# Kernel optimization log

Hardware: AMD Instinct MI355X
Metric: run time of the kernel (lower is better)

## Reference

```python
import jax, jax.numpy as jnp
import numpy as np

# wav2vec2 feature-extractor conv stack config: (kernel, stride) per layer, 512 channels
CONV_CFG = [(10, 5), (3, 2), (3, 2), (3, 2), (3, 2), (2, 2), (2, 2)]
C = 512
PROJ = 256
HID = 128
NCLS = 5
N_WORDS = 64
B = 8
L = 40000


def _conv1d(h, w, stride):
    # h: [B, Cin, T], w: [Cout, Cin, K]
    return jax.lax.conv_general_dilated(
        h, w, window_strides=(stride,), padding='VALID',
        dimension_numbers=('NCH', 'OIH', 'NCH'))


def setup_inputs() -> dict:
    key = jax.random.key(0)
    ks = jax.random.split(key, 16)
    x = jax.random.normal(ks[0], (B, L), dtype=jnp.float32)
    word_ids = jax.random.randint(ks[1], (B,), 0, N_WORDS)
    convs = {}
    cin = 1
    for i, (k, s) in enumerate(CONV_CFG):
        fan = cin * k
        convs[f'conv{i}'] = jax.random.normal(ks[2 + i], (C, cin, k), dtype=jnp.float32) / np.sqrt(fan)
        cin = C
    gn_scale = jnp.ones((C,), dtype=jnp.float32)
    gn_bias = jnp.zeros((C,), dtype=jnp.float32)
    proj_w = jax.random.normal(ks[9], (PROJ, C), dtype=jnp.float32) / np.sqrt(C)
    proj_b = jnp.zeros((PROJ,), dtype=jnp.float32)
    cls_w1 = jax.random.normal(ks[10], (N_WORDS, PROJ, HID), dtype=jnp.float32) / np.sqrt(PROJ)
    cls_b1 = jnp.zeros((N_WORDS, HID), dtype=jnp.float32)
    cls_w2 = jax.random.normal(ks[11], (N_WORDS, HID, NCLS), dtype=jnp.float32) / np.sqrt(HID)
    cls_b2 = jnp.zeros((N_WORDS, NCLS), dtype=jnp.float32)
    return dict(x=x, word_ids=word_ids, gn_scale=gn_scale, gn_bias=gn_bias,
                proj_w=proj_w, proj_b=proj_b, cls_w1=cls_w1, cls_b1=cls_b1,
                cls_w2=cls_w2, cls_b2=cls_b2, **convs)


def _forward(x, convs, gn_scale, gn_bias, proj_w, proj_b, cls_w1, cls_b1, cls_w2, cls_b2, word_ids):
    h = x[:, None, :]  # [B,1,L]
    for i, (k, s) in enumerate(CONV_CFG):
        h = _conv1d(h, convs[i], s)
        if i == 0:
            # wav2vec2 group-norm: groups == channels -> per-channel norm over time
            mu = jnp.mean(h, axis=-1, keepdims=True)
            var = jnp.var(h, axis=-1, keepdims=True)
            h = (h - mu) * jax.lax.rsqrt(var + 1e-5)
            h = h * gn_scale[None, :, None] + gn_bias[None, :, None]
        h = jax.nn.gelu(h)
    feat = jnp.mean(h, axis=-1)                          # [B, 512] mean-pool over time
    feat = jax.nn.relu(feat @ proj_w.T + proj_b)         # [B, 256] (dropout = identity in eval)
    w1 = cls_w1[word_ids]                                # [B, 256, 128] routed gather
    h1 = jax.nn.relu(jnp.einsum('bd,bdh->bh', feat, w1) + cls_b1[word_ids])
    out = jnp.einsum('bh,bho->bo', h1, cls_w2[word_ids]) + cls_b2[word_ids]  # [B, 5]
    return out


def reference(x, word_ids, gn_scale, gn_bias, proj_w, proj_b, cls_w1, cls_b1, cls_w2, cls_b2,
              conv0, conv1, conv2, conv3, conv4, conv5, conv6):
    convs = [conv0, conv1, conv2, conv3, conv4, conv5, conv6]
    return _forward(x, convs, gn_scale, gn_bias, proj_w, proj_b,
                    cls_w1, cls_b1, cls_w2, cls_b2, word_ids)
```

## Files before the change

### kernel.cpp

```cpp
#include <hip/hip_runtime.h>
#include <hip/hip_bf16.h>

typedef unsigned short u16;
typedef short bf16x8 __attribute__((ext_vector_type(8)));
typedef float f32x4 __attribute__((ext_vector_type(4)));

#define CC 512

__device__ __forceinline__ float gelu_tanh(float x) {
    float x3 = x * x * x;
    float z  = 0.7978845608028654f * (x + 0.044715f * x3);
    float e  = __expf(2.0f * z);
    float th = 1.0f - 2.0f / (e + 1.0f);
    return 0.5f * x * (1.0f + th);
}

__device__ __forceinline__ u16 f2bf(float f) {
    union { float f; unsigned u; } v; v.f = f;
    unsigned r = v.u + 0x7fff + ((v.u >> 16) & 1);
    return (u16)(r >> 16);
}
__device__ __forceinline__ float bf2f(u16 h) {
    union { unsigned u; float f; } v; v.u = ((unsigned)h) << 16; return v.f;
}

__global__ __launch_bounds__(256) void conv0_stats(
    const float* __restrict__ x, const float* __restrict__ w0,
    float* __restrict__ part) {
    const int chunk = blockIdx.x, b = blockIdx.y;
    const int t0 = chunk * 250;
    __shared__ float xs[250 * 5 + 10];
    __shared__ float w0s[512 * 10];
    for (int i = threadIdx.x; i < 1260; i += 256) {
        int gi = t0 * 5 + i;
        xs[i] = (gi < 40000) ? x[b * 40000 + gi] : 0.0f;
    }
    for (int i = threadIdx.x; i < 5120; i += 256) w0s[i] = w0[i];
    __syncthreads();
    const int nt = min(250, 7999 - t0);
    for (int cc = 0; cc < 2; ++cc) {
        const int c = threadIdx.x * 2 + cc;
        const float* wr = &w0s[c * 10];
        float s = 0.0f, q = 0.0f;
        for (int t = 0; t < nt; ++t) {
            float a = 0.0f;
#pragma unroll
            for (int j = 0; j < 10; ++j) a = fmaf(wr[j], xs[t * 5 + j], a);
            s += a; q += a * a;
        }
        float* p = part + ((size_t)(b * 512 + c) * 32 + chunk) * 2;
        p[0] = s; p[1] = q;
    }
}

__global__ __launch_bounds__(256) void stats_finalize(
    const float* __restrict__ part, float* __restrict__ stats) {
    const int row = blockIdx.x * 256 + threadIdx.x;
    const float* p = part + (size_t)row * 32 * 2;
    float s = 0.0f, q = 0.0f;
    for (int k = 0; k < 32; ++k) { s += p[k * 2]; q += p[k * 2 + 1]; }
    float mean = s / 7999.0f;
    float var  = fmaxf(q / 7999.0f - mean * mean, 0.0f);
    stats[row * 2]     = mean;
    stats[row * 2 + 1] = rsqrtf(var + 1e-5f);
}

__global__ __launch_bounds__(256) void conv0_apply(
    const float* __restrict__ x, const float* __restrict__ w0,
    const float* __restrict__ stats, const float* __restrict__ gsc,
    const float* __restrict__ gbi, u16* __restrict__ actG) {
    const int t0 = blockIdx.x * 32, b = blockIdx.y;
    __shared__ float xs[32 * 5 + 16];
    __shared__ float w0s[512 * 10];
    __shared__ float A[512], Bb[512];
    for (int i = threadIdx.x; i < 170; i += 256) {
        int gi = t0 * 5 + i;
        xs[i] = (gi < 40000) ? x[b * 40000 + gi] : 0.0f;
    }
    for (int i = threadIdx.x; i < 5120; i += 256) w0s[i] = w0[i];
    for (int c = threadIdx.x; c < 512; c += 256) {
        float m = stats[(b * 512 + c) * 2], r = stats[(b * 512 + c) * 2 + 1];
        float a = r * gsc[c];
        A[c] = a; Bb[c] = gbi[c] - m * a;
    }
    __syncthreads();
    const int c0 = (threadIdx.x & 63) * 8;
    const int wv = threadIdx.x >> 6;
    u16 res[8][8];
#pragma unroll
    for (int q = 0; q < 8; ++q) {
        const int c = c0 + q;
        float wreg[10];
#pragma unroll
        for (int j = 0; j < 10; ++j) wreg[j] = w0s[c * 10 + j];
        const float Ar = A[c], Br = Bb[c];
#pragma unroll
        for (int u = 0; u < 8; ++u) {
            const int tt = wv * 8 + u;
            float a = 0.0f;
#pragma unroll
            for (int j = 0; j < 10; ++j) a = fmaf(wreg[j], xs[tt * 5 + j], a);
            res[u][q] = f2bf(gelu_tanh(fmaf(a, Ar, Br)));
        }
    }
#pragma unroll
    for (int u = 0; u < 8; ++u) {
        const int t = t0 + wv * 8 + u;
        union { u16 s[8]; uint4 v; } pk;
#pragma unroll
        for (int q = 0; q < 8; ++q) pk.s[q] = (t < 7999) ? res[u][q] : (u16)0;
        *(uint4*)(actG + ((size_t)b * 8320 + t) * 512 + c0) = pk.v;
    }
}

template <int K, int NL>
struct WtBatch { const float* src[NL]; u16* dst[NL]; };

template <int K, int NL>
__global__ __launch_bounds__(256) void wt_transform(WtBatch<K, NL> a) {
    constexpr int WROW = 32 * K + 8;
    const int cit = blockIdx.x, cob = blockIdx.y, l = blockIdx.z;
    const float* w = a.src[l];
    u16* dst = a.dst[l] + ((size_t)(cob * 16 + cit)) * 128 * WROW;
    for (int idx = threadIdx.x; idx < 128 * WROW; idx += 256) {
        const int co = idx / WROW, e = idx - co * WROW;
        u16 hi = 0;
        if (e < 32 * K) {
            const int j = e >> 5, ci = e & 31;
            hi = f2bf(w[((size_t)(cob * 128 + co) * 512 + cit * 32 + ci) * K + j]);
        }
        dst[idx] = hi;
    }
}

template <int K, int TT>
__global__ __launch_bounds__(256, (TT == 128 ? 2 : 3)) void conv_mfma(
    const u16* __restrict__ act, int capIn,
    const u16* __restrict__ wt,
    u16* __restrict__ outAct, int capOut, int tbShift) {
    constexpr int WROW = 32 * K + 8;
    constexpr int XH   = TT + 8;
    constexpr int TF   = TT / 32;
    constexpr int NXCH = XH * 8;
    constexpr int NWCH = 128 * WROW / 8;

    __shared__ __align__(16) u16 Xs[XH * 64];
    __shared__ __align__(16) u16 Ws[128 * WROW];

    const int tid  = threadIdx.x;
    const int lane = tid & 63;
    const int wv   = tid >> 6;
    const int wco  = wv >> 1, wtt = wv & 1;
    const int l15  = lane & 15, l16 = lane >> 4;

    const int flat = blockIdx.x;
    const int xcd  = flat & 7, cob = (flat >> 3) & 3;
    const int G    = xcd + (flat >> 5) * 8;
    const int t_b  = G & ((1 << tbShift) - 1);
    const int b    = G >> tbShift;
    const int t0   = t_b * TT;
    const int x0   = t0 * 2;

    const char* abase = (const char*)(act + (size_t)b * capIn * 512);
    const u16*  wbase = wt + (size_t)cob * (16 * 128 * WROW);

    auto stageX = [&](int cit) {
        const char* asl = abase + cit * 64;
#pragma unroll
        for (int k = 0; k < (NXCH + 255) / 256; ++k) {
            const int cb = wv * 64 + k * 256;
            if (cb < NXCH) {
                const int c  = cb + lane;
                const int xh = c >> 3;
                const int li = ((c & 7) * 16) ^ ((xh & 7) << 4);
                int x = x0 + 2 * xh + (li >> 6);
                x = min(x, capIn - 1);
                __builtin_amdgcn_global_load_lds(
                    (const __attribute__((address_space(1))) void*)(asl + (size_t)x * 1024 + (li & 63)),
                    (__attribute__((address_space(3))) void*)((char*)&Xs[0] + cb * 16),
                    16, 0, 0);
            }
        }
    };
    auto stageW = [&](int cit) {
        const char* p = (const char*)(wbase + (size_t)cit * 128 * WROW);
#pragma unroll
        for (int k = 0; k < (NWCH + 255) / 256; ++k) {
            const int cb = wv * 64 + k * 256;
            if (cb < NWCH)
                __builtin_amdgcn_global_load_lds(
                    (const __attribute__((address_space(1))) void*)(p + (size_t)(cb + lane) * 16),
                    (__attribute__((address_space(3))) void*)((char*)&Ws[0] + cb * 16),
                    16, 0, 0);
        }
    };

    int xoff[K][TF];
    int woff[K][4];
#pragma unroll
    for (int j = 0; j < K; ++j) {
#pragma unroll
        for (int tf = 0; tf < TF; ++tf) {
            const int tl = wtt * (TT / 2) + tf * 16 + l15;
            const int xl = 2 * tl + j;
            const int xh = xl >> 1, p = xl & 1;
            xoff[j][tf] = xh * 128 + ((p * 64 + l16 * 16) ^ ((xh & 7) << 4));
        }
#pragma unroll
        for (int cf = 0; cf < 4; ++cf)
            woff[j][cf] = (wco * 64 + cf * 16 + l15) * WROW + j * 32 + l16 * 8;
    }

    f32x4 acc[4][TF] = {};

    stageX(0); stageW(0);
    __syncthreads();

#pragma unroll 1
    for (int cit = 0; cit < 16; ++cit) {
        bf16x8 xr[K][TF], wr[K][4];
#pragma unroll
        for (int j = 0; j < K; ++j) {
#pragma unroll
            for (int tf = 0; tf < TF; ++tf)
                xr[j][tf] = *(const bf16x8*)((const char*)&Xs[0] + xoff[j][tf]);
#pragma unroll
            for (int cf = 0; cf < 4; ++cf)
                wr[j][cf] = *(const bf16x8*)(&Ws[0] + woff[j][cf]);
        }
        __syncthreads();
        if (cit < 15) { stageX(cit + 1); stageW(cit + 1); }
#pragma unroll
        for (int j = 0; j < K; ++j)
#pragma unroll
            for (int cf = 0; cf < 4; ++cf)
#pragma unroll
                for (int tf = 0; tf < TF; ++tf)
                    acc[cf][tf] = __builtin_amdgcn_mfma_f32_16x16x32_bf16(
                        wr[j][cf], xr[j][tf], acc[cf][tf], 0, 0, 0);
        __syncthreads();
    }

    u16* ob = outAct + (size_t)b * capOut * 512;
#pragma unroll
    for (int cf = 0; cf < 4; ++cf) {
#pragma unroll
        for (int tf = 0; tf < TF; ++tf) {
            const int tG  = t0 + wtt * (TT / 2) + tf * 16 + l15;
            const int coG = cob * 128 + wco * 64 + cf * 16 + l16 * 4;
            union { u16 s[4]; uint2 v; } pk;
#pragma unroll
            for (int r = 0; r < 4; ++r)
                pk.s[r] = f2bf(gelu_tanh(acc[cf][tf][r]));
            *(uint2*)(ob + (size_t)tG * 512 + coG) = pk.v;
        }
    }
}

__global__ __launch_bounds__(512) void feat_proj_kernel(
    const u16* __restrict__ act, int cap,
    const float* __restrict__ pw, const float* __restrict__ pb,
    float* __restrict__ pfeat) {
    const int b = blockIdx.x;
    __shared__ float feat[CC];
    const int c = threadIdx.x;
    float s = 0.0f;
    for (int t = 0; t < 124; ++t) s += bf2f(act[((size_t)b * cap + t) * 512 + c]);
    feat[c] = s * (1.0f / 124.0f);
    __syncthreads();
    if (threadIdx.x < 256) {
        const int j = threadIdx.x;
        const float* wr = pw + (size_t)j * CC;
        float acc = pb[j];
        for (int cc = 0; cc < CC; ++cc) acc = fmaf(feat[cc], wr[cc], acc);
        pfeat[b * 256 + j] = fmaxf(acc, 0.0f);
    }
}

__global__ __launch_bounds__(128) void cls_kernel(
    const float* __restrict__ pfeat, const int* __restrict__ wid,
    const float* __restrict__ w1, const float* __restrict__ b1,
    const float* __restrict__ w2, const float* __restrict__ b2,
    float* __restrict__ out) {
    const int b = blockIdx.x;
    const int id = wid[b];
    __shared__ float pf[256], h1[128];
    for (int d = threadIdx.x; d < 256; d += 128) pf[d] = pfeat[b * 256 + d];
    __syncthreads();
    {
        const int hh = threadIdx.x;
        const float* w1p = w1 + (size_t)id * 256 * 128;
        float s = b1[id * 128 + hh];
        for (int d = 0; d < 256; ++d) s = fmaf(pf[d], w1p[d * 128 + hh], s);
        h1[hh] = fmaxf(s, 0.0f);
    }
    __syncthreads();
    if (threadIdx.x < 5) {
        const float* w2p = w2 + (size_t)id * 128 * 5;
        float s = b2[id * 5 + threadIdx.x];
        for (int hh = 0; hh < 128; ++hh) s = fmaf(h1[hh], w2p[hh * 5 + threadIdx.x], s);
        out[b * 5 + threadIdx.x] = s;
    }
}

extern "C" void kernel_launch(void* const* d_in, const int* in_sizes, int n_in,
                              void* d_out, int out_size, void* d_ws, size_t ws_size,
                              hipStream_t stream) {
    const float* x   = (const float*)d_in[0];
    const int*   wid = (const int*)d_in[1];
    const float* gsc = (const float*)d_in[2];
    const float* gbi = (const float*)d_in[3];
    const float* pw  = (const float*)d_in[4];
    const float* pb  = (const float*)d_in[5];
    const float* w1  = (const float*)d_in[6];
    const float* b1  = (const float*)d_in[7];
    const float* w2  = (const float*)d_in[8];
    const float* b2  = (const float*)d_in[9];
    const float* cw[7];
    for (int i = 0; i < 7; ++i) cw[i] = (const float*)d_in[10 + i];

    char* ws = (char*)d_ws;
    const size_t SZ_ACTG = (size_t)8 * 8320 * 512 * 2;
    const size_t SZ_P    = (size_t)8 * 4224 * 512 * 2;
    const size_t SZ_Q    = (size_t)8 * 2176 * 512 * 2;
    u16* actG = (u16*)ws;
    u16* bufP = (u16*)(ws + SZ_ACTG);
    u16* bufQ = (u16*)(ws + SZ_ACTG + SZ_P);
    size_t off = SZ_ACTG + SZ_P + SZ_Q;
    u16* wtbuf[7];
    for (int i = 1; i <= 4; ++i) { wtbuf[i] = (u16*)(ws + off); off += (size_t)4 * 16 * 128 * 104 * 2; }
    for (int i = 5; i <= 6; ++i) { wtbuf[i] = (u16*)(ws + off); off += (size_t)4 * 16 * 128 * 72 * 2; }
    off = (off + 255) & ~(size_t)255;
    float* statsPart = (float*)(ws + off); off += (size_t)4096 * 32 * 2 * 4;
    float* stats     = (float*)(ws + off); off += 4096 * 2 * 4;
    float* pfeat     = (float*)(ws + off); off += 8 * 256 * 4;

    conv0_stats<<<dim3(32, 8), 256, 0, stream>>>(x, cw[0], statsPart);
    stats_finalize<<<dim3(16), 256, 0, stream>>>(statsPart, stats);
    conv0_apply<<<dim3(260, 8), 256, 0, stream>>>(x, cw[0], stats, gsc, gbi, actG);

    {
        WtBatch<3, 4> a;
        for (int i = 0; i < 4; ++i) { a.src[i] = cw[1 + i]; a.dst[i] = wtbuf[1 + i]; }
        wt_transform<3, 4><<<dim3(16, 4, 4), 256, 0, stream>>>(a);
        WtBatch<2, 2> c;
        for (int i = 0; i < 2; ++i) { c.src[i] = cw[5 + i]; c.dst[i] = wtbuf[5 + i]; }
        wt_transform<2, 2><<<dim3(16, 4, 2), 256, 0, stream>>>(c);
    }

    conv_mfma<3, 128><<<dim3(32 * 32), 256, 0, stream>>>(actG, 8320, wtbuf[1], bufP, 4224, 5);
    conv_mfma<3, 128><<<dim3(16 * 32), 256, 0, stream>>>(bufP, 4224, wtbuf[2], bufQ, 2176, 4);
    conv_mfma<3,  64><<<dim3(16 * 32), 256, 0, stream>>>(bufQ, 2176, wtbuf[3], bufP, 4224, 4);
    conv_mfma<3,  64><<<dim3( 8 * 32), 256, 0, stream>>>(bufP, 4224, wtbuf[4], bufQ, 2176, 3);
    conv_mfma<2,  64><<<dim3( 4 * 32), 256, 0, stream>>>(bufQ, 2176, wtbuf[5], bufP, 4224, 2);
    conv_mfma<2,  64><<<dim3( 2 * 32), 256, 0, stream>>>(bufP, 4224, wtbuf[6], bufQ, 2176, 1);

    feat_proj_kernel<<<dim3(8), 512, 0, stream>>>(bufQ, 2176, pw, pb, pfeat);
    cls_kernel<<<dim3(8), 128, 0, stream>>>(pfeat, wid, w1, b1, w2, b2, (float*)d_out);
}
```

Measured before the change: 347.6 us.

## Store raw conv0 output once, then compute group-norm stats and apply from memory

Conv0 previously ran twice: once to accumulate per-channel statistics and once to recompute the convolution and apply the norm and GELU. Now it is computed once and stored as bf16. Separate kernels then read that buffer to build the statistics, fold scale and bias into A/B coefficients, and apply norm plus GELU in place. This trades the duplicate conv compute for extra passes over a roughly 65 MB activation buffer, and the statistics are taken from bf16-rounded values. The launch-bounds occupancy hints for conv_mfma are also raised.

```diff
diff --git a/kernel.cpp b/kernel.cpp
--- a/kernel.cpp
+++ b/kernel.cpp
@@ -24,93 +24,99 @@
     union { unsigned u; float f; } v; v.u = ((unsigned)h) << 16; return v.f;
 }
 
-__global__ __launch_bounds__(256) void conv0_stats(
+__global__ __launch_bounds__(256) void conv0_store(
     const float* __restrict__ x, const float* __restrict__ w0,
-    float* __restrict__ part) {
+    u16* __restrict__ actG) {
+    const int t0 = blockIdx.x * 64, b = blockIdx.y;
+    __shared__ float xs[64 * 5 + 16];
+    __shared__ float w0t[10 * 512];
+    for (int i = threadIdx.x; i < 64 * 5 + 5; i += 256) {
+        int gi = t0 * 5 + i;
+        xs[i] = (gi < 40000) ? x[b * 40000 + gi] : 0.0f;
+    }
+    for (int i = threadIdx.x; i < 5120; i += 256) {
+        int c = i / 10, j = i - c * 10;
+        w0t[j * 512 + c] = w0[i];
+    }
+    __syncthreads();
+    const int lane = threadIdx.x & 63, wv = threadIdx.x >> 6;
+    float wr[8][10];
+#pragma unroll
+    for (int q = 0; q < 8; ++q)
+#pragma unroll
+        for (int j = 0; j < 10; ++j) wr[q][j] = w0t[j * 512 + lane + 64 * q];
+    u16* ob = actG + ((size_t)b * 8320 + t0 + wv * 16) * 512 + lane;
+#pragma unroll
+    for (int u = 0; u < 16; ++u) {
+        const int tt = wv * 16 + u;
+        float xv[10];
+#pragma unroll
+        for (int j = 0; j < 10; ++j) xv[j] = xs[tt * 5 + j];
+#pragma unroll
+        for (int q = 0; q < 8; ++q) {
+            float a = 0.0f;
+#pragma unroll
+            for (int j = 0; j < 10; ++j) a = fmaf(wr[q][j], xv[j], a);
+            ob[(size_t)u * 512 + 64 * q] = f2bf(a);
+        }
+    }
+}
+
+__global__ __launch_bounds__(256) void gn_stats2(
+    const u16* __restrict__ actG, float* __restrict__ part) {
     const int chunk = blockIdx.x, b = blockIdx.y;
     const int t0 = chunk * 250;
-    __shared__ float xs[250 * 5 + 10];
-    __shared__ float w0s[512 * 10];
-    for (int i = threadIdx.x; i < 1260; i += 256) {
-        int gi = t0 * 5 + i;
-        xs[i] = (gi < 40000) ? x[b * 40000 + gi] : 0.0f;
-    }
-    for (int i = threadIdx.x; i < 5120; i += 256) w0s[i] = w0[i];
-    __syncthreads();
     const int nt = min(250, 7999 - t0);
-    for (int cc = 0; cc < 2; ++cc) {
-        const int c = threadIdx.x * 2 + cc;
-        const float* wr = &w0s[c * 10];
-        float s = 0.0f, q = 0.0f;
-        for (int t = 0; t < nt; ++t) {
-            float a = 0.0f;
-#pragma unroll
-            for (int j = 0; j < 10; ++j) a = fmaf(wr[j], xs[t * 5 + j], a);
-            s += a; q += a * a;
-        }
-        float* p = part + ((size_t)(b * 512 + c) * 32 + chunk) * 2;
-        p[0] = s; p[1] = q;
-    }
-}
-
-__global__ __launch_bounds__(256) void stats_finalize(
-    const float* __restrict__ part, float* __restrict__ stats) {
+    float s0 = 0, q0 = 0, s1 = 0, q1 = 0;
+    const u16* base = actG + ((size_t)b * 8320 + t0) * 512;
+    for (int t = 0; t < nt; ++t) {
+        float v0 = bf2f(base[(size_t)t * 512 + threadIdx.x]);
+        float v1 = bf2f(base[(size_t)t * 512 + 256 + threadIdx.x]);
+        s0 += v0; q0 += v0 * v0;
+        s1 += v1; q1 += v1 * v1;
+    }
+    float* p0 = part + ((size_t)(b * 512 + threadIdx.x) * 32 + chunk) * 2;
+    p0[0] = s0; p0[1] = q0;
+    float* p1 = part + ((size_t)(b * 512 + 256 + threadIdx.x) * 32 + chunk) * 2;
+    p1[0] = s1; p1[1] = q1;
+}
+
+__global__ __launch_bounds__(256) void stats_finalizeAB(
+    const float* __restrict__ part, const float* __restrict__ gsc,
+    const float* __restrict__ gbi, float* __restrict__ Af, float* __restrict__ Bf) {
     const int row = blockIdx.x * 256 + threadIdx.x;
     const float* p = part + (size_t)row * 32 * 2;
     float s = 0.0f, q = 0.0f;
     for (int k = 0; k < 32; ++k) { s += p[k * 2]; q += p[k * 2 + 1]; }
     float mean = s / 7999.0f;
     float var  = fmaxf(q / 7999.0f - mean * mean, 0.0f);
-    stats[row * 2]     = mean;
-    stats[row * 2 + 1] = rsqrtf(var + 1e-5f);
-}
-
-__global__ __launch_bounds__(256) void conv0_apply(
-    const float* __restrict__ x, const float* __restrict__ w0,
-    const float* __restrict__ stats, const float* __restrict__ gsc,
-    const float* __restrict__ gbi, u16* __restrict__ actG) {
-    const int t0 = blockIdx.x * 32, b = blockIdx.y;
-    __shared__ float xs[32 * 5 + 16];
-    __shared__ float w0s[512 * 10];
-    __shared__ float A[512], Bb[512];
-    for (int i = threadIdx.x; i < 170; i += 256) {
-        int gi = t0 * 5 + i;
-        xs[i] = (gi < 40000) ? x[b * 40000 + gi] : 0.0f;
-    }
-    for (int i = threadIdx.x; i < 5120; i += 256) w0s[i] = w0[i];
-    for (int c = threadIdx.x; c < 512; c += 256) {
-        float m = stats[(b * 512 + c) * 2], r = stats[(b * 512 + c) * 2 + 1];
-        float a = r * gsc[c];
-        A[c] = a; Bb[c] = gbi[c] - m * a;
-    }
-    __syncthreads();
-    const int c0 = (threadIdx.x & 63) * 8;
-    const int wv = threadIdx.x >> 6;
-    u16 res[8][8];
-#pragma unroll
-    for (int q = 0; q < 8; ++q) {
-        const int c = c0 + q;
-        float wreg[10];
-#pragma unroll
-        for (int j = 0; j < 10; ++j) wreg[j] = w0s[c * 10 + j];
-        const float Ar = A[c], Br = Bb[c];
-#pragma unroll
-        for (int u = 0; u < 8; ++u) {
-            const int tt = wv * 8 + u;
-            float a = 0.0f;
-#pragma unroll
-            for (int j = 0; j < 10; ++j) a = fmaf(wreg[j], xs[tt * 5 + j], a);
-            res[u][q] = f2bf(gelu_tanh(fmaf(a, Ar, Br)));
-        }
-    }
-#pragma unroll
-    for (int u = 0; u < 8; ++u) {
-        const int t = t0 + wv * 8 + u;
-        union { u16 s[8]; uint4 v; } pk;
-#pragma unroll
-        for (int q = 0; q < 8; ++q) pk.s[q] = (t < 7999) ? res[u][q] : (u16)0;
-        *(uint4*)(actG + ((size_t)b * 8320 + t) * 512 + c0) = pk.v;
-    }
+    float rstd = rsqrtf(var + 1e-5f);
+    const int c = row & (CC - 1);
+    float A = rstd * gsc[c];
+    Af[row] = A;
+    Bf[row] = gbi[c] - mean * A;
+}
+
+__global__ __launch_bounds__(256) void gn_apply(
+    u16* __restrict__ actG, const float* __restrict__ Af,
+    const float* __restrict__ Bf) {
+    const int b = blockIdx.y;
+    const int idx = blockIdx.x * 256 + threadIdx.x;
+    const int row = idx >> 6, c0 = (idx & 63) * 8;
+    if (row >= 7999) return;
+    u16* p = actG + ((size_t)b * 8320 + row) * 512 + c0;
+    union { u16 s[8]; uint4 v; } in, outv;
+    in.v = *(const uint4*)p;
+    const float4 a0 = *(const float4*)(Af + b * 512 + c0);
+    const float4 a1 = *(const float4*)(Af + b * 512 + c0 + 4);
+    const float4 b0 = *(const float4*)(Bf + b * 512 + c0);
+    const float4 b1 = *(const float4*)(Bf + b * 512 + c0 + 4);
+    const float av[8] = {a0.x, a0.y, a0.z, a0.w, a1.x, a1.y, a1.z, a1.w};
+    const float bv[8] = {b0.x, b0.y, b0.z, b0.w, b1.x, b1.y, b1.z, b1.w};
+#pragma unroll
+    for (int e = 0; e < 8; ++e)
+        outv.s[e] = f2bf(gelu_tanh(fmaf(bf2f(in.s[e]), av[e], bv[e])));
+    *(uint4*)p = outv.v;
 }
 
 template <int K, int NL>
@@ -134,7 +140,7 @@
 }
 
 template <int K, int TT>
-__global__ __launch_bounds__(256, (TT == 128 ? 2 : 3)) void conv_mfma(
+__global__ __launch_bounds__(256, (TT == 128 ? 3 : 4)) void conv_mfma(
     const u16* __restrict__ act, int capIn,
     const u16* __restrict__ wt,
     u16* __restrict__ outAct, int capOut, int tbShift) {
@@ -332,12 +338,14 @@
     for (int i = 5; i <= 6; ++i) { wtbuf[i] = (u16*)(ws + off); off += (size_t)4 * 16 * 128 * 72 * 2; }
     off = (off + 255) & ~(size_t)255;
     float* statsPart = (float*)(ws + off); off += (size_t)4096 * 32 * 2 * 4;
-    float* stats     = (float*)(ws + off); off += 4096 * 2 * 4;
+    float* Af        = (float*)(ws + off); off += 4096 * 4;
+    float* Bf        = (float*)(ws + off); off += 4096 * 4;
     float* pfeat     = (float*)(ws + off); off += 8 * 256 * 4;
 
-    conv0_stats<<<dim3(32, 8), 256, 0, stream>>>(x, cw[0], statsPart);
-    stats_finalize<<<dim3(16), 256, 0, stream>>>(statsPart, stats);
-    conv0_apply<<<dim3(260, 8), 256, 0, stream>>>(x, cw[0], stats, gsc, gbi, actG);
+    conv0_store<<<dim3(125, 8), 256, 0, stream>>>(x, cw[0], actG);
+    gn_stats2<<<dim3(32, 8), 256, 0, stream>>>(actG, statsPart);
+    stats_finalizeAB<<<dim3(16), 256, 0, stream>>>(statsPart, gsc, gbi, Af, Bf);
+    gn_apply<<<dim3(2000, 8), 256, 0, stream>>>(actG, Af, Bf);
 
     {
         WtBatch<3, 4> a;
```

New measurement: 627.5 us. 1.8x slower.
